# Kernel tuning notes

Measured on AMD Instinct MI355X. Metric: run time of the kernel, lower is better.

## Reference

```python
import jax, jax.numpy as jnp
import numpy as np

EPS = 1e-5
INF = 1e9
H, D = 8, 32  # no_heads = c_m/32, c_hidden = 32


def rmsnorm(x, w, eps=EPS):
    return x * jax.lax.rsqrt(jnp.mean(x * x, axis=-1, keepdims=True) + eps) * w


def setup_inputs() -> dict:
    key = jax.random.key(0)
    ks = jax.random.split(key, 10)
    B, S, c_m, c_z = 64, 512, 256, 128
    sc_m = 1.0 / np.sqrt(c_m)
    sc_z = 1.0 / np.sqrt(c_z)
    return {
        "m": jax.random.normal(ks[0], (B, S, c_m), jnp.float32),
        "z": jax.random.normal(ks[1], (S, S, c_z), jnp.float32),
        "z_mask": jnp.ones((S, S), jnp.float32),
        "w_norm_m": jnp.ones((c_m,), jnp.float32),
        "w_norm_z": jnp.ones((c_z,), jnp.float32),
        "Wq": jax.random.normal(ks[2], (c_m, c_m), jnp.float32) * sc_m,
        "Wk": jax.random.normal(ks[3], (c_m, c_m), jnp.float32) * sc_m,
        "Wv": jax.random.normal(ks[4], (c_m, c_m), jnp.float32) * sc_m,
        "Wz": jax.random.normal(ks[5], (c_z, H), jnp.float32) * sc_z,
        "Wg": jax.random.normal(ks[6], (c_m, c_m), jnp.float32) * sc_m,
        "bg": jnp.zeros((c_m,), jnp.float32),
        "Wo": jax.random.normal(ks[7], (c_m, c_m), jnp.float32) * sc_m,
        "bo": jnp.zeros((c_m,), jnp.float32),
    }


def reference(m, z, z_mask, w_norm_m, w_norm_z, Wq, Wk, Wv, Wz, Wg, bg, Wo, bo):
    B, S, c_m = m.shape
    m_norm = rmsnorm(m, w_norm_m)   # [B,S,c_m]
    z_norm = rmsnorm(z, w_norm_z)   # [S,S,c_z]

    q = (m_norm @ Wq).reshape(B, S, H, D)  # [B,S,H,D]
    k = (m_norm @ Wk).reshape(B, S, H, D)
    v = (m_norm @ Wv).reshape(B, S, H, D)
    g = m_norm @ Wg + bg                   # [B,S,c_m]

    # pair bias: [S,S,H] -> [H,S,S], plus additive mask (-inf where z_mask == 0)
    pair_bias = jnp.einsum('ijc,ch->hij', z_norm, Wz)          # [H,S,S]
    mask_bias = jnp.where(z_mask > 0, 0.0, -INF).astype(q.dtype)  # [S,S]
    bias = pair_bias[None] + mask_bias[None, None]             # [1,H,S,S]

    scale = 1.0 / np.sqrt(D)
    scores = jnp.einsum('bqhd,bkhd->bhqk', q, k) * scale + bias  # [B,H,S,S]
    attn = jax.nn.softmax(scores, axis=-1)
    out = jnp.einsum('bhqk,bkhd->bqhd', attn, v).reshape(B, S, c_m)

    o = (out @ Wo + bo) * g
    return o.astype(jnp.float32)
```

## Files before the change

### kernel.cpp

```cpp
#include <hip/hip_runtime.h>

typedef short bf16x8 __attribute__((ext_vector_type(8)));
typedef float f32x4 __attribute__((ext_vector_type(4)));

#define DI __device__ __forceinline__

#define LOG2E 1.44269504088896f
#define QSCALE (0.17677669529663687f * 1.44269504088896f)

static DI unsigned short f2bf(float f) {
  union { float f; unsigned u; } v; v.f = f;
  unsigned r = v.u + 0x7FFFu + ((v.u >> 16) & 1u);
  return (unsigned short)(r >> 16);
}

static DI unsigned cvt_pk_bf16(float lo, float hi) {
  unsigned r;
  asm("v_cvt_pk_bf16_f32 %0, %1, %2" : "=v"(r) : "v"(lo), "v"(hi));
  return r;
}

static DI float bflo(unsigned u) { return __uint_as_float(u << 16); }
static DI float bfhi(unsigned u) { return __uint_as_float(u & 0xffff0000u); }

static DI void gld16(const void* g, void* l) {
  __builtin_amdgcn_global_load_lds((__attribute__((address_space(1))) void*)g,
                                   (__attribute__((address_space(3))) void*)l,
                                   16, 0, 0);
}

__global__ __launch_bounds__(256) void k_cast_weights(
    const float* __restrict__ Wq, const float* __restrict__ Wk,
    const float* __restrict__ Wv, const float* __restrict__ Wg,
    const float* __restrict__ Wo,
    unsigned short* __restrict__ Wt_qkvg, unsigned short* __restrict__ Wt_o) {
  int t = blockIdx.x * 256 + threadIdx.x;
  if (t < 262144) {
    int n = t & 1023, kk = t >> 10;
    const float* W = (n < 256) ? Wq : (n < 512) ? Wk : (n < 768) ? Wv : Wg;
    Wt_qkvg[(size_t)n * 256 + kk] = f2bf(W[kk * 256 + (n & 255)]);
  } else if (t < 262144 + 65536) {
    int u = t - 262144;
    int n = u & 255, kk = u >> 8;
    int h = kk >> 5, e = kk & 31;
    int d = (e >> 1) + ((e & 1) << 4);
    Wt_o[n * 256 + kk] = f2bf(Wo[(h * 32 + d) * 256 + n]);
  }
}

__global__ __launch_bounds__(256) void k_rmsnorm_m(
    const float* __restrict__ m, const float* __restrict__ w,
    unsigned short* __restrict__ m_norm) {
  int wave = threadIdx.x >> 6, lane = threadIdx.x & 63;
  int row = blockIdx.x * 4 + wave;
  const float4 x = *(const float4*)(m + (size_t)row * 256 + lane * 4);
  float ss = x.x * x.x + x.y * x.y + x.z * x.z + x.w * x.w;
#pragma unroll
  for (int mk = 1; mk < 64; mk <<= 1) ss += __shfl_xor(ss, mk, 64);
  float rms = rsqrtf(ss * (1.0f / 256.0f) + 1e-5f);
  const float4 wv = *(const float4*)(w + lane * 4);
  ushort4 o;
  o.x = f2bf(x.x * rms * wv.x);
  o.y = f2bf(x.y * rms * wv.y);
  o.z = f2bf(x.z * rms * wv.z);
  o.w = f2bf(x.w * rms * wv.w);
  *(ushort4*)(m_norm + (size_t)row * 256 + lane * 4) = o;
}

__global__ __launch_bounds__(256) void k_pair_bias(
    const float* __restrict__ z, const float* __restrict__ z_mask,
    const float* __restrict__ w_norm_z, const float* __restrict__ Wz,
    unsigned* __restrict__ biasf) {
  int gw = blockIdx.x * 4 + (threadIdx.x >> 6);
  int lane = threadIdx.x & 63;
  int half = lane >> 5, li = lane & 31;
  f32x4 wzl[4], wzh[4];
#pragma unroll
  for (int i = 0; i < 4; ++i) {
    wzl[i] = *(const f32x4*)(Wz + (li * 4 + i) * 8);
    wzh[i] = *(const f32x4*)(Wz + (li * 4 + i) * 8 + 4);
  }
  const float4 wn = *(const float4*)(w_norm_z + li * 4);

  for (int it = 0; it < 8; ++it) {
    int p = it * 16384 + gw;
    int i = p >> 8, jp = p & 255;
    int j = jp * 2 + half;
    int rr = i * 512 + j;
    const float4 a = *(const float4*)(z + (size_t)rr * 128 + li * 4);
    float mb = (z_mask[rr] > 0.0f) ? 0.0f : -1e9f;

    float ss = a.x * a.x + a.y * a.y + a.z * a.z + a.w * a.w;
#pragma unroll
    for (int mk = 1; mk < 32; mk <<= 1) ss += __shfl_xor(ss, mk, 64);
    float rms = rsqrtf(ss * (1.0f / 128.0f) + 1e-5f);

    float y0 = a.x * wn.x, y1 = a.y * wn.y, y2 = a.z * wn.z, y3 = a.w * wn.w;
    f32x4 pl = y0 * wzl[0] + y1 * wzl[1] + y2 * wzl[2] + y3 * wzl[3];
    f32x4 ph = y0 * wzh[0] + y1 * wzh[1] + y2 * wzh[2] + y3 * wzh[3];

    int b0 = li & 1, b1 = (li >> 1) & 1, b2 = (li >> 2) & 1;
    float A[4] = {pl[0], pl[2], ph[0], ph[2]};
    float Bv[4] = {pl[1], pl[3], ph[1], ph[3]};
    float keep[4];
#pragma unroll
    for (int i2 = 0; i2 < 4; ++i2) {
      float send = b0 ? A[i2] : Bv[i2];
      float recv = __shfl_xor(send, 1, 64);
      keep[i2] = (b0 ? Bv[i2] : A[i2]) + recv;
    }
    float s2x = b1 ? keep[0] : keep[1];
    float s2y = b1 ? keep[2] : keep[3];
    float r2x = __shfl_xor(s2x, 2, 64);
    float r2y = __shfl_xor(s2y, 2, 64);
    float k2x = (b1 ? keep[1] : keep[0]) + r2x;
    float k2y = (b1 ? keep[3] : keep[2]) + r2y;
    float s3 = b2 ? k2x : k2y;
    float r3 = __shfl_xor(s3, 4, 64);
    float fin = (b2 ? k2y : k2x) + r3;
    fin += __shfl_xor(fin, 8, 64);
    fin += __shfl_xor(fin, 16, 64);

    float full = (fin * rms + mb) * LOG2E;
    float fo = __shfl_xor(full, 32, 64);
    if (half == 0 && li < 8) {
      unsigned pk = cvt_pk_bf16(full, fo);
      int j0 = jp * 2;
      int l = (i & 15) + 16 * ((j0 & 15) >> 2);
      size_t o = ((((size_t)li * 32 + (i >> 4)) * 32 + (j0 >> 4)) * 64 + l) * 2 +
                 ((jp) & 1);
      biasf[o] = pk;
    }
  }
}

DI void gemm_mainloop_g(const unsigned short* a0, const unsigned short* a1,
                        const unsigned short* b0, const unsigned short* b1,
                        size_t Astep, unsigned short* At, unsigned short* Bts,
                        f32x4 acc[4][4]) {
  int tid = threadIdx.x, lane = tid & 63, w = tid >> 6;
  int wm = w >> 1, wn = w & 1;
  int r16 = lane & 15, g = lane >> 4;
  int gx = (g ^ ((r16 >> 1) & 3)) * 8;
  unsigned short* lA0 = At + w * 1024;
  unsigned short* lA1 = At + w * 1024 + 512;
  unsigned short* lB0 = Bts + w * 1024;
  unsigned short* lB1 = Bts + w * 1024 + 512;
  for (int ks = 0; ks < 8; ++ks) {
    gld16(a0 + ks * Astep, lA0);
    gld16(a1 + ks * Astep, lA1);
    gld16(b0 + ks * 32, lB0);
    gld16(b1 + ks * 32, lB1);
    __syncthreads();
    bf16x8 af[4], bfr[4];
#pragma unroll
    for (int i = 0; i < 4; ++i)
      af[i] = *(const bf16x8*)(At + (wm * 64 + i * 16 + r16) * 32 + gx);
#pragma unroll
    for (int j = 0; j < 4; ++j)
      bfr[j] = *(const bf16x8*)(Bts + (wn * 64 + j * 16 + r16) * 32 + gx);
#pragma unroll
    for (int i = 0; i < 4; ++i)
#pragma unroll
      for (int j = 0; j < 4; ++j)
        acc[i][j] = __builtin_amdgcn_mfma_f32_16x16x32_bf16(af[i], bfr[j],
                                                            acc[i][j], 0, 0, 0);
    __syncthreads();
  }
}

__global__ __launch_bounds__(256) void k_gemm_qkvg(
    const unsigned short* __restrict__ m_norm, const unsigned short* __restrict__ Wt,
    const float* __restrict__ bg,
    unsigned short* __restrict__ q_ws, unsigned short* __restrict__ k_ws,
    unsigned short* __restrict__ v_ws, float* __restrict__ g_ws) {
  __shared__ unsigned short At[4096];
  __shared__ unsigned short Bts[4096];
  int mb = blockIdx.x * 128, nb = blockIdx.y * 128;
  int tid = threadIdx.x, lane = tid & 63, w = tid >> 6;
  int c0 = w * 128 + lane, c1 = c0 + 64;
  int row0 = c0 >> 2, q0 = (c0 & 3) ^ ((row0 >> 1) & 3);
  int row1 = c1 >> 2, q1 = (c1 & 3) ^ ((row1 >> 1) & 3);
  f32x4 acc[4][4] = {};
  gemm_mainloop_g(m_norm + (size_t)(mb + row0) * 256 + q0 * 8,
                  m_norm + (size_t)(mb + row1) * 256 + q1 * 8,
                  Wt + (size_t)(nb + row0) * 256 + q0 * 8,
                  Wt + (size_t)(nb + row1) * 256 + q1 * 8,
                  32, At, Bts, acc);
  int wm = w >> 1, wn = w & 1;
  int r16 = lane & 15, rg = lane >> 4;
#pragma unroll
  for (int i = 0; i < 4; ++i)
#pragma unroll
    for (int j = 0; j < 4; ++j) {
      int n = nb + wn * 64 + j * 16 + r16;
#pragma unroll
      for (int r = 0; r < 4; ++r) {
        int mrow = mb + wm * 64 + i * 16 + rg * 4 + r;
        int bb = mrow >> 9, s = mrow & 511;
        float v = acc[i][j][r];
        if (n < 768) {
          int tsel = n >> 8, hh = (n >> 5) & 7, dd = n & 31;
          unsigned short* dst = (tsel == 0) ? q_ws : (tsel == 1) ? k_ws : v_ws;
          float vv = (tsel == 0) ? v * QSCALE : v;
          dst[(((size_t)bb * 8 + hh) * 512 + s) * 32 + dd] = f2bf(vv);
        } else {
          int n2 = n & 255;
          g_ws[(size_t)mrow * 256 + n2] = v + bg[n2];
        }
      }
    }
}

__global__ __launch_bounds__(256) void k_gemm_out(
    const unsigned short* __restrict__ attn, const unsigned short* __restrict__ Wt_o,
    const float* __restrict__ bo, const float* __restrict__ g_ws,
    float* __restrict__ out) {
  __shared__ unsigned short At[4096];
  __shared__ unsigned short Bts[4096];
  int mb = blockIdx.x * 128, nb = blockIdx.y * 128;
  int tid = threadIdx.x, lane = tid & 63, w = tid >> 6;
  int c0 = w * 128 + lane, c1 = c0 + 64;
  int row0 = c0 >> 2, q0 = (c0 & 3) ^ ((row0 >> 1) & 3);
  int row1 = c1 >> 2, q1 = (c1 & 3) ^ ((row1 >> 1) & 3);
  int mrow0 = mb + row0, mrow1 = mb + row1;
  f32x4 acc[4][4] = {};
  gemm_mainloop_g(
      attn + ((size_t)(mrow0 >> 9) * 8) * 16384 + (size_t)(mrow0 & 511) * 32 + q0 * 8,
      attn + ((size_t)(mrow1 >> 9) * 8) * 16384 + (size_t)(mrow1 & 511) * 32 + q1 * 8,
      Wt_o + (size_t)(nb + row0) * 256 + q0 * 8,
      Wt_o + (size_t)(nb + row1) * 256 + q1 * 8,
      16384, At, Bts, acc);
  int wm = w >> 1, wn = w & 1;
  int r16 = lane & 15, rg = lane >> 4;
#pragma unroll
  for (int i = 0; i < 4; ++i)
#pragma unroll
    for (int j = 0; j < 4; ++j) {
      int n = nb + wn * 64 + j * 16 + r16;
#pragma unroll
      for (int r = 0; r < 4; ++r) {
        int mrow = mb + wm * 64 + i * 16 + rg * 4 + r;
        out[(size_t)mrow * 256 + n] = (acc[i][j][r] + bo[n]) * g_ws[(size_t)mrow * 256 + n];
      }
    }
}

#define VT_LD 522
__global__ __launch_bounds__(256, 2) void k_attn(
    const unsigned short* __restrict__ q_ws, const unsigned short* __restrict__ k_ws,
    const unsigned short* __restrict__ v_ws, const unsigned* __restrict__ biasf,
    unsigned short* __restrict__ attn_out) {
  __shared__ unsigned short Vt[32 * VT_LD];
  int tid = threadIdx.x;
  int wave = tid >> 6, lane = tid & 63;
  int bx = blockIdx.x;
  int quarter = bx >> 9, h = (bx >> 6) & 7, b = bx & 63;
  size_t base = ((size_t)b * 8 + h) * (512 * 32);
  const unsigned short* qb = q_ws + base;
  const unsigned short* kb = k_ws + base;
  const unsigned short* vb = v_ws + base;
#pragma unroll
  for (int it = 0; it < 8; ++it) {
    int idx = it * 256 + tid;
    int s = idx >> 2, kk = idx & 3, d0 = kk * 8;
    bf16x8 vv = *(const bf16x8*)(vb + s * 32 + d0);
    int col = (s & ~31) + ((s >> 2) & 3) * 8 + ((s >> 4) & 1) * 4 + (s & 3);
#pragma unroll
    for (int j = 0; j < 8; ++j) Vt[(d0 + j) * VT_LD + col] = (unsigned short)vv[j];
  }
  __syncthreads();

  int r16 = lane & 15, g = lane >> 4;
  const unsigned* bh_ = biasf + (size_t)h * 131072 + lane * 2;
  unsigned short* ob = attn_out + base;
  const f32x4 zero = {0.f, 0.f, 0.f, 0.f};

  for (int qt = 0; qt < 2; ++qt) {
    int qbase = quarter * 128 + (wave * 2 + qt) * 16;
    const unsigned* bq = bh_ + (size_t)(qbase >> 4) * 4096;
    bf16x8 qf = *(const bf16x8*)(qb + (qbase + r16) * 32 + g * 8);
    f32x4 o0 = zero, o1 = zero;
    float smA = 0.f, smB = 0.f, smC = 0.f, smD = 0.f;
#pragma unroll
    for (int c = 0; c < 16; ++c) {
      bf16x8 kf0 = *(const bf16x8*)(kb + ((c * 2) * 16 + r16) * 32 + g * 8);
      bf16x8 kf1 = *(const bf16x8*)(kb + ((c * 2 + 1) * 16 + r16) * 32 + g * 8);
      uint2 u0 = *(const uint2*)(bq + (c * 2) * 128);
      uint2 u1 = *(const uint2*)(bq + (c * 2 + 1) * 128);
      __builtin_amdgcn_s_setprio(1);
      f32x4 s0 = __builtin_amdgcn_mfma_f32_16x16x32_bf16(kf0, qf, zero, 0, 0, 0);
      f32x4 s1 = __builtin_amdgcn_mfma_f32_16x16x32_bf16(kf1, qf, zero, 0, 0, 0);
      __builtin_amdgcn_s_setprio(0);
      s0[0] += bflo(u0.x); s0[1] += bfhi(u0.x);
      s0[2] += bflo(u0.y); s0[3] += bfhi(u0.y);
      s1[0] += bflo(u1.x); s1[1] += bfhi(u1.x);
      s1[2] += bflo(u1.y); s1[3] += bfhi(u1.y);
#pragma unroll
      for (int r = 0; r < 4; ++r) {
        s0[r] = exp2f(s0[r]);
        s1[r] = exp2f(s1[r]);
      }
      smA += s0[0] + s1[0];
      smB += s0[1] + s1[1];
      smC += s0[2] + s1[2];
      smD += s0[3] + s1[3];
      union { unsigned u[4]; bf16x8 v; } pa;
      pa.u[0] = cvt_pk_bf16(s0[0], s0[1]);
      pa.u[1] = cvt_pk_bf16(s0[2], s0[3]);
      pa.u[2] = cvt_pk_bf16(s1[0], s1[1]);
      pa.u[3] = cvt_pk_bf16(s1[2], s1[3]);
      bf16x8 vf0 = *(const bf16x8*)(Vt + r16 * VT_LD + c * 32 + g * 8);
      bf16x8 vf1 = *(const bf16x8*)(Vt + (r16 + 16) * VT_LD + c * 32 + g * 8);
      __builtin_amdgcn_s_setprio(1);
      o0 = __builtin_amdgcn_mfma_f32_16x16x32_bf16(pa.v, vf0, o0, 0, 0, 0);
      o1 = __builtin_amdgcn_mfma_f32_16x16x32_bf16(pa.v, vf1, o1, 0, 0, 0);
      __builtin_amdgcn_s_setprio(0);
    }
    float S = smA + smB + smC + smD;
    S += __shfl_xor(S, 16, 64);
    S += __shfl_xor(S, 32, 64);
    float invS = 1.0f / S;
#pragma unroll
    for (int r = 0; r < 4; ++r) {
      float ir = __int_as_float(
          __builtin_amdgcn_ds_bpermute((4 * g + r) * 4, __float_as_int(invS)));
      int s = qbase + g * 4 + r;
      unsigned pk = cvt_pk_bf16(o0[r] * ir, o1[r] * ir);
      *(unsigned*)(ob + (size_t)s * 32 + r16 * 2) = pk;
    }
  }
}

extern "C" void kernel_launch(void* const* d_in, const int* in_sizes, int n_in,
                              void* d_out, int out_size, void* d_ws, size_t ws_size,
                              hipStream_t stream) {
  (void)in_sizes; (void)n_in; (void)out_size; (void)ws_size;
  const float* m        = (const float*)d_in[0];
  const float* z        = (const float*)d_in[1];
  const float* z_mask   = (const float*)d_in[2];
  const float* w_norm_m = (const float*)d_in[3];
  const float* w_norm_z = (const float*)d_in[4];
  const float* Wq = (const float*)d_in[5];
  const float* Wk = (const float*)d_in[6];
  const float* Wv = (const float*)d_in[7];
  const float* Wz = (const float*)d_in[8];
  const float* Wg = (const float*)d_in[9];
  const float* bg = (const float*)d_in[10];
  const float* Wo = (const float*)d_in[11];
  const float* bo = (const float*)d_in[12];
  float* out = (float*)d_out;

  char* ws = (char*)d_ws;
  size_t off = 0;
  unsigned short* m_norm  = (unsigned short*)(ws + off); off += (size_t)32768 * 256 * 2;
  unsigned short* Wt_qkvg = (unsigned short*)(ws + off); off += (size_t)1024 * 256 * 2;
  unsigned short* Wt_o    = (unsigned short*)(ws + off); off += (size_t)256 * 256 * 2;
  unsigned short* q_ws    = (unsigned short*)(ws + off); off += (size_t)64 * 8 * 512 * 32 * 2;
  unsigned short* k_ws    = (unsigned short*)(ws + off); off += (size_t)64 * 8 * 512 * 32 * 2;
  unsigned short* v_ws    = (unsigned short*)(ws + off); off += (size_t)64 * 8 * 512 * 32 * 2;
  float* g_ws             = (float*)(ws + off);          off += (size_t)32768 * 256 * 4;
  unsigned* biasf         = (unsigned*)(ws + off);       off += (size_t)8 * 32 * 32 * 128 * 4;
  unsigned short* attn_out = m_norm;

  hipLaunchKernelGGL(k_cast_weights, dim3(1280), dim3(256), 0, stream,
                     Wq, Wk, Wv, Wg, Wo, Wt_qkvg, Wt_o);
  hipLaunchKernelGGL(k_rmsnorm_m, dim3(8192), dim3(256), 0, stream, m, w_norm_m, m_norm);
  hipLaunchKernelGGL(k_pair_bias, dim3(4096), dim3(256), 0, stream,
                     z, z_mask, w_norm_z, Wz, biasf);
  hipLaunchKernelGGL(k_gemm_qkvg, dim3(256, 8), dim3(256), 0, stream,
                     m_norm, Wt_qkvg, bg, q_ws, k_ws, v_ws, g_ws);
  hipLaunchKernelGGL(k_attn, dim3(2048), dim3(256), 0, stream,
                     q_ws, k_ws, v_ws, biasf, attn_out);
  hipLaunchKernelGGL(k_gemm_out, dim3(256, 2), dim3(256), 0, stream,
                     attn_out, Wt_o, bo, g_ws, out);
}
```

Baseline: 179.4 us.

## Double-buffer LDS tiles in GEMM mainloop to overlap loads with MFMA

The shared GEMM mainloop used by the QKVG projection and output projection kernels now keeps two LDS buffers. It issues the global-to-LDS loads for the next K-slice before running the MFMAs on the current one, which removes one barrier per iteration. The aim is to hide global load latency behind matrix math. In exchange it doubles the LDS footprint per block, which may lower occupancy. The GEMMs are only a part of the total kernel time.

Result: slower. 189.5 us (+5.6%).

```diff
diff --git a/kernel.cpp b/kernel.cpp
--- a/kernel.cpp
+++ b/kernel.cpp
@@ -134,6 +134,23 @@
   }
 }
 
+DI void gemm_compute32(const unsigned short* cA, const unsigned short* cB,
+                       int wm, int wn, int r16, int gx, f32x4 acc[4][4]) {
+  bf16x8 af[4], bfr[4];
+#pragma unroll
+  for (int i = 0; i < 4; ++i)
+    af[i] = *(const bf16x8*)(cA + (wm * 64 + i * 16 + r16) * 32 + gx);
+#pragma unroll
+  for (int j = 0; j < 4; ++j)
+    bfr[j] = *(const bf16x8*)(cB + (wn * 64 + j * 16 + r16) * 32 + gx);
+#pragma unroll
+  for (int i = 0; i < 4; ++i)
+#pragma unroll
+    for (int j = 0; j < 4; ++j)
+      acc[i][j] = __builtin_amdgcn_mfma_f32_16x16x32_bf16(af[i], bfr[j],
+                                                          acc[i][j], 0, 0, 0);
+}
+
 DI void gemm_mainloop_g(const unsigned short* a0, const unsigned short* a1,
                         const unsigned short* b0, const unsigned short* b1,
                         size_t Astep, unsigned short* At, unsigned short* Bts,
@@ -142,31 +159,25 @@
   int wm = w >> 1, wn = w & 1;
   int r16 = lane & 15, g = lane >> 4;
   int gx = (g ^ ((r16 >> 1) & 3)) * 8;
-  unsigned short* lA0 = At + w * 1024;
-  unsigned short* lA1 = At + w * 1024 + 512;
-  unsigned short* lB0 = Bts + w * 1024;
-  unsigned short* lB1 = Bts + w * 1024 + 512;
-  for (int ks = 0; ks < 8; ++ks) {
-    gld16(a0 + ks * Astep, lA0);
-    gld16(a1 + ks * Astep, lA1);
-    gld16(b0 + ks * 32, lB0);
-    gld16(b1 + ks * 32, lB1);
+  unsigned short* lA = At + w * 1024;
+  unsigned short* lB = Bts + w * 1024;
+  gld16(a0, lA);
+  gld16(a1, lA + 512);
+  gld16(b0, lB);
+  gld16(b1, lB + 512);
+  __syncthreads();
+  int cur = 0;
+  for (int ks = 0; ks < 7; ++ks) {
+    int nxt = cur ^ 1;
+    gld16(a0 + (ks + 1) * Astep, lA + nxt * 4096);
+    gld16(a1 + (ks + 1) * Astep, lA + nxt * 4096 + 512);
+    gld16(b0 + (ks + 1) * 32, lB + nxt * 4096);
+    gld16(b1 + (ks + 1) * 32, lB + nxt * 4096 + 512);
+    gemm_compute32(At + cur * 4096, Bts + cur * 4096, wm, wn, r16, gx, acc);
     __syncthreads();
-    bf16x8 af[4], bfr[4];
-#pragma unroll
-    for (int i = 0; i < 4; ++i)
-      af[i] = *(const bf16x8*)(At + (wm * 64 + i * 16 + r16) * 32 + gx);
-#pragma unroll
-    for (int j = 0; j < 4; ++j)
-      bfr[j] = *(const bf16x8*)(Bts + (wn * 64 + j * 16 + r16) * 32 + gx);
-#pragma unroll
-    for (int i = 0; i < 4; ++i)
-#pragma unroll
-      for (int j = 0; j < 4; ++j)
-        acc[i][j] = __builtin_amdgcn_mfma_f32_16x16x32_bf16(af[i], bfr[j],
-                                                            acc[i][j], 0, 0, 0);
-    __syncthreads();
-  }
+    cur = nxt;
+  }
+  gemm_compute32(At + cur * 4096, Bts + cur * 4096, wm, wn, r16, gx, acc);
 }
 
 __global__ __launch_bounds__(256) void k_gemm_qkvg(
@@ -174,8 +185,8 @@
     const float* __restrict__ bg,
     unsigned short* __restrict__ q_ws, unsigned short* __restrict__ k_ws,
     unsigned short* __restrict__ v_ws, float* __restrict__ g_ws) {
-  __shared__ unsigned short At[4096];
-  __shared__ unsigned short Bts[4096];
+  __shared__ unsigned short At[8192];
+  __shared__ unsigned short Bts[8192];
   int mb = blockIdx.x * 128, nb = blockIdx.y * 128;
   int tid = threadIdx.x, lane = tid & 63, w = tid >> 6;
   int c0 = w * 128 + lane, c1 = c0 + 64;
@@ -216,8 +227,8 @@
     const unsigned short* __restrict__ attn, const unsigned short* __restrict__ Wt_o,
     const float* __restrict__ bo, const float* __restrict__ g_ws,
     float* __restrict__ out) {
-  __shared__ unsigned short At[4096];
-  __shared__ unsigned short Bts[4096];
+  __shared__ unsigned short At[8192];
+  __shared__ unsigned short Bts[8192];
   int mb = blockIdx.x * 128, nb = blockIdx.y * 128;
   int tid = threadIdx.x, lane = tid & 63, w = tid >> 6;
   int c0 = w * 128 + lane, c1 = c0 + 64;
```

## Merge weight cast with rmsnorm and interleave pair-bias blocks into QKVG GEMM launch

Applied to the files above, without the earlier changes.

Weight casting and m-rmsnorm now run as one launch split by block index. The pair-bias computation is folded into the QKVG GEMM launch, with two pair-bias blocks interleaved per GEMM block, so the memory-bound z pass overlaps the compute-bound GEMM. This removes two launches and the idle tail between independent stages. In exchange, the LDS and register footprint of the GEMM now applies to the pair-bias blocks too, which can lower their occupancy.

Result: slower. 221.4 us (+23.4%).

```diff
diff --git a/kernel.cpp b/kernel.cpp
--- a/kernel.cpp
+++ b/kernel.cpp
@@ -29,36 +29,37 @@
                                    16, 0, 0);
 }
 
-__global__ __launch_bounds__(256) void k_cast_weights(
+__global__ __launch_bounds__(256) void k_prep(
     const float* __restrict__ Wq, const float* __restrict__ Wk,
     const float* __restrict__ Wv, const float* __restrict__ Wg,
     const float* __restrict__ Wo,
-    unsigned short* __restrict__ Wt_qkvg, unsigned short* __restrict__ Wt_o) {
-  int t = blockIdx.x * 256 + threadIdx.x;
-  if (t < 262144) {
-    int n = t & 1023, kk = t >> 10;
-    const float* W = (n < 256) ? Wq : (n < 512) ? Wk : (n < 768) ? Wv : Wg;
-    Wt_qkvg[(size_t)n * 256 + kk] = f2bf(W[kk * 256 + (n & 255)]);
-  } else if (t < 262144 + 65536) {
-    int u = t - 262144;
-    int n = u & 255, kk = u >> 8;
-    int h = kk >> 5, e = kk & 31;
-    int d = (e >> 1) + ((e & 1) << 4);
-    Wt_o[n * 256 + kk] = f2bf(Wo[(h * 32 + d) * 256 + n]);
-  }
-}
-
-__global__ __launch_bounds__(256) void k_rmsnorm_m(
-    const float* __restrict__ m, const float* __restrict__ w,
+    unsigned short* __restrict__ Wt_qkvg, unsigned short* __restrict__ Wt_o,
+    const float* __restrict__ m, const float* __restrict__ w_norm_m,
     unsigned short* __restrict__ m_norm) {
+  int bx = blockIdx.x;
+  if (bx < 1280) {
+    int t = bx * 256 + threadIdx.x;
+    if (t < 262144) {
+      int n = t & 1023, kk = t >> 10;
+      const float* W = (n < 256) ? Wq : (n < 512) ? Wk : (n < 768) ? Wv : Wg;
+      Wt_qkvg[(size_t)n * 256 + kk] = f2bf(W[kk * 256 + (n & 255)]);
+    } else if (t < 262144 + 65536) {
+      int u = t - 262144;
+      int n = u & 255, kk = u >> 8;
+      int h = kk >> 5, e = kk & 31;
+      int d = (e >> 1) + ((e & 1) << 4);
+      Wt_o[n * 256 + kk] = f2bf(Wo[(h * 32 + d) * 256 + n]);
+    }
+    return;
+  }
   int wave = threadIdx.x >> 6, lane = threadIdx.x & 63;
-  int row = blockIdx.x * 4 + wave;
+  int row = (bx - 1280) * 4 + wave;
   const float4 x = *(const float4*)(m + (size_t)row * 256 + lane * 4);
   float ss = x.x * x.x + x.y * x.y + x.z * x.z + x.w * x.w;
 #pragma unroll
   for (int mk = 1; mk < 64; mk <<= 1) ss += __shfl_xor(ss, mk, 64);
   float rms = rsqrtf(ss * (1.0f / 256.0f) + 1e-5f);
-  const float4 wv = *(const float4*)(w + lane * 4);
+  const float4 wv = *(const float4*)(w_norm_m + lane * 4);
   ushort4 o;
   o.x = f2bf(x.x * rms * wv.x);
   o.y = f2bf(x.y * rms * wv.y);
@@ -67,11 +68,12 @@
   *(ushort4*)(m_norm + (size_t)row * 256 + lane * 4) = o;
 }
 
-__global__ __launch_bounds__(256) void k_pair_bias(
-    const float* __restrict__ z, const float* __restrict__ z_mask,
-    const float* __restrict__ w_norm_z, const float* __restrict__ Wz,
-    unsigned* __restrict__ biasf) {
-  int gw = blockIdx.x * 4 + (threadIdx.x >> 6);
+DI void pair_bias_body(int pbx, const float* __restrict__ z,
+                       const float* __restrict__ z_mask,
+                       const float* __restrict__ w_norm_z,
+                       const float* __restrict__ Wz,
+                       unsigned* __restrict__ biasf) {
+  int gw = pbx * 4 + (threadIdx.x >> 6);
   int lane = threadIdx.x & 63;
   int half = lane >> 5, li = lane & 31;
   f32x4 wzl[4], wzh[4];
@@ -169,14 +171,24 @@
   }
 }
 
-__global__ __launch_bounds__(256) void k_gemm_qkvg(
+__global__ __launch_bounds__(256) void k_gemm_qkvg_pair(
     const unsigned short* __restrict__ m_norm, const unsigned short* __restrict__ Wt,
     const float* __restrict__ bg,
     unsigned short* __restrict__ q_ws, unsigned short* __restrict__ k_ws,
-    unsigned short* __restrict__ v_ws, float* __restrict__ g_ws) {
+    unsigned short* __restrict__ v_ws, float* __restrict__ g_ws,
+    const float* __restrict__ z, const float* __restrict__ z_mask,
+    const float* __restrict__ w_norm_z, const float* __restrict__ Wz,
+    unsigned* __restrict__ biasf) {
   __shared__ unsigned short At[4096];
   __shared__ unsigned short Bts[4096];
-  int mb = blockIdx.x * 128, nb = blockIdx.y * 128;
+  int bx = blockIdx.x;
+  int q3 = bx / 3, r3 = bx - q3 * 3;
+  if (r3 != 0) {
+    pair_bias_body(q3 * 2 + (r3 - 1), z, z_mask, w_norm_z, Wz, biasf);
+    return;
+  }
+  int gidx = q3;
+  int mb = (gidx & 255) * 128, nb = (gidx >> 8) * 128;
   int tid = threadIdx.x, lane = tid & 63, w = tid >> 6;
   int c0 = w * 128 + lane, c1 = c0 + 64;
   int row0 = c0 >> 2, q0 = (c0 & 3) ^ ((row0 >> 1) & 3);
@@ -363,13 +375,11 @@
   unsigned* biasf         = (unsigned*)(ws + off);       off += (size_t)8 * 32 * 32 * 128 * 4;
   unsigned short* attn_out = m_norm;
 
-  hipLaunchKernelGGL(k_cast_weights, dim3(1280), dim3(256), 0, stream,
-                     Wq, Wk, Wv, Wg, Wo, Wt_qkvg, Wt_o);
-  hipLaunchKernelGGL(k_rmsnorm_m, dim3(8192), dim3(256), 0, stream, m, w_norm_m, m_norm);
-  hipLaunchKernelGGL(k_pair_bias, dim3(4096), dim3(256), 0, stream,
+  hipLaunchKernelGGL(k_prep, dim3(9472), dim3(256), 0, stream,
+                     Wq, Wk, Wv, Wg, Wo, Wt_qkvg, Wt_o, m, w_norm_m, m_norm);
+  hipLaunchKernelGGL(k_gemm_qkvg_pair, dim3(6144), dim3(256), 0, stream,
+                     m_norm, Wt_qkvg, bg, q_ws, k_ws, v_ws, g_ws,
                      z, z_mask, w_norm_z, Wz, biasf);
-  hipLaunchKernelGGL(k_gemm_qkvg, dim3(256, 8), dim3(256), 0, stream,
-                     m_norm, Wt_qkvg, bg, q_ws, k_ws, v_ws, g_ws);
   hipLaunchKernelGGL(k_attn, dim3(2048), dim3(256), 0, stream,
                      q_ws, k_ws, v_ws, biasf, attn_out);
   hipLaunchKernelGGL(k_gemm_out, dim3(256, 2), dim3(256), 0, stream,
```
